# Performance work log

Measured on AMD Instinct MI355X. Metric: run time of the kernel, lower is better.

The kernel has to match this reference:

```python
import jax, jax.numpy as jnp
import numpy as np

N_EMBD = 1024
BLOCK_SIZE = 2048
ATTN_SPAN = 256
LN_EPS = 1e-5


def _band_mask(T, span, dtype):
    ones = jnp.ones((T, T), dtype=dtype)
    # tril(.,0) * (1 - tril(.,-span)) -> causal band of width `span`
    return jnp.tril(ones, 0) * (1.0 - jnp.tril(ones, -span))


def setup_inputs() -> dict:
    key = jax.random.key(0)
    k_x, k_w, k_b, k_lw = jax.random.split(key, 4)
    B, T, C = 4, BLOCK_SIZE, N_EMBD
    x = jax.random.normal(k_x, (B, T, C), dtype=jnp.float32)
    # qkv_net: Linear(C, 3C) with bias (torch default)
    lim = 1.0 / np.sqrt(C)
    W_qkv = jax.random.uniform(k_w, (C, 3 * C), minval=-lim, maxval=lim, dtype=jnp.float32)
    b_qkv = jax.random.uniform(k_b, (3 * C,), minval=-lim, maxval=lim, dtype=jnp.float32)
    ln_w = jnp.ones((C,), dtype=jnp.float32)
    ln_b = jnp.zeros((C,), dtype=jnp.float32)
    return {"x": x, "W_qkv": W_qkv, "b_qkv": b_qkv, "ln_w": ln_w, "ln_b": ln_b}


def _layer_norm(h, w, b):
    mu = jnp.mean(h, axis=-1, keepdims=True)
    var = jnp.var(h, axis=-1, keepdims=True)
    return (h - mu) * jax.lax.rsqrt(var + LN_EPS) * w + b


def reference(x, W_qkv, b_qkv, ln_w, ln_b):
    B, T, C = x.shape
    qkv = x @ W_qkv + b_qkv  # [B,T,3C]
    q, k, v = jnp.split(qkv, 3, axis=-1)
    scale = np.sqrt(C * ATTN_SPAN).astype(np.float32)
    scores = jnp.einsum('bid,bjd->bij', q, k) / scale  # [B,T,T]
    scores = scores * _band_mask(T, ATTN_SPAN, x.dtype)[None, :, :]
    out = jnp.einsum('bij,bjd->bid', scores, v)  # [B,T,C]
    return _layer_norm(out, ln_w, ln_b)
```

## Files before the change

kernel.cpp:

```cpp
#include <hip/hip_runtime.h>
#include <cstdint>
#include <cstddef>

#define N_EMBD 1024
#define T_SEQ  2048
#define NBATCH 4
#define SPAN   256
#define C3     3072

typedef float  floatx4 __attribute__((ext_vector_type(4)));
typedef __bf16 bf16x8  __attribute__((ext_vector_type(8)));

__device__ inline unsigned short f2bf(float f) {
    union { float f; unsigned u; } x; x.f = f;
    unsigned u = x.u;
    unsigned r = (u + 0x7fffu + ((u >> 16) & 1u)) >> 16;
    return (unsigned short)r;
}

typedef __attribute__((address_space(1))) const void GVOID;
typedef __attribute__((address_space(3))) void LVOID;
__device__ inline void gl2lds16(const void* g, void* l) {
    __builtin_amdgcn_global_load_lds((GVOID*)g, (LVOID*)l, 16, 0, 0);
}

__device__ inline void stage128x32(const unsigned short* g, size_t stride,
                                   unsigned short* lds, int lane, int wave) {
    const int r     = wave * 16 + (lane >> 2);
    const int chunk = (lane & 3) ^ ((lane >> 3) & 3);
    const unsigned short* src = g + (size_t)r * stride + chunk * 8;
    gl2lds16(src,               &lds[(wave * 16) * 32]);
    gl2lds16(src + 64 * stride, &lds[(64 + wave * 16) * 32]);
}

__global__ __launch_bounds__(256) void k_prep(const float* __restrict__ x,
                                              unsigned short* __restrict__ Xb,
                                              const float* __restrict__ W,
                                              unsigned short* __restrict__ WbT) {
    __shared__ unsigned short t[32][33];
    if (blockIdx.x < 8192) {
        int i = (blockIdx.x * 256 + threadIdx.x) * 4;
        float4 v = *(const float4*)(x + i);
        ushort4 o;
        o.x = f2bf(v.x); o.y = f2bf(v.y); o.z = f2bf(v.z); o.w = f2bf(v.w);
        *(ushort4*)(Xb + i) = o;
    } else {
        int bid = blockIdx.x - 8192;
        int k0 = (bid & 31) * 32, n0 = (bid >> 5) * 32;
        int tx = threadIdx.x & 31, ty = threadIdx.x >> 5;
#pragma unroll
        for (int i = 0; i < 4; i++) {
            int k = k0 + ty + i * 8;
            t[ty + i * 8][tx] = f2bf(W[(size_t)k * C3 + n0 + tx]);
        }
        __syncthreads();
#pragma unroll
        for (int i = 0; i < 4; i++) {
            int n = n0 + ty + i * 8;
            WbT[(size_t)n * N_EMBD + k0 + tx] = t[tx][ty + i * 8];
        }
    }
}

__global__ __launch_bounds__(256) void k_qkv_gemm(const unsigned short* __restrict__ Xb,
                                                  const unsigned short* __restrict__ WbT,
                                                  const float* __restrict__ bqkv,
                                                  unsigned short* __restrict__ QK,
                                                  unsigned short* __restrict__ Vt) {
    __shared__ unsigned short smem[17408];
    unsigned short* As = smem;
    unsigned short* Bs = smem + 4096;
    const int tid = threadIdx.x, lane = tid & 63, wave = tid >> 6;
    const int n0 = blockIdx.x * 128, m0 = blockIdx.y * 128;
    const int wr = wave >> 1, wc = wave & 1;

    floatx4 acc[4][4] = {};

    const unsigned short* gA = Xb  + (size_t)m0 * N_EMBD;
    const unsigned short* gB = WbT + (size_t)n0 * N_EMBD;
    const int qk = ((lane >> 4) ^ ((lane >> 1) & 3)) * 8;
    const int ra = wr * 64 + (lane & 15);
    const int rb = wc * 64 + (lane & 15);

    for (int k0 = 0; k0 < N_EMBD; k0 += 32) {
        stage128x32(gA + k0, N_EMBD, As, lane, wave);
        stage128x32(gB + k0, N_EMBD, Bs, lane, wave);
        __syncthreads();
        bf16x8 a[4], b[4];
#pragma unroll
        for (int mi = 0; mi < 4; mi++) a[mi] = *(const bf16x8*)&As[(ra + mi * 16) * 32 + qk];
#pragma unroll
        for (int ni = 0; ni < 4; ni++) b[ni] = *(const bf16x8*)&Bs[(rb + ni * 16) * 32 + qk];
#pragma unroll
        for (int mi = 0; mi < 4; mi++)
#pragma unroll
            for (int ni = 0; ni < 4; ni++)
                acc[mi][ni] = __builtin_amdgcn_mfma_f32_16x16x32_bf16(a[mi], b[ni], acc[mi][ni], 0, 0, 0);
        __syncthreads();
    }

    const int cn = lane & 15, q = lane >> 4;
    if (n0 < 2048) {
#pragma unroll
        for (int ni = 0; ni < 4; ni++) {
            const int n = n0 + wc * 64 + ni * 16 + cn;
            const float bias = bqkv[n];
#pragma unroll
            for (int mi = 0; mi < 4; mi++) {
                const int mbase = m0 + wr * 64 + mi * 16 + q * 4;
#pragma unroll
                for (int r = 0; r < 4; r++)
                    QK[(size_t)(mbase + r) * 2048 + n] = f2bf(acc[mi][ni][r] + bias);
            }
        }
    } else {
        unsigned short* tp = smem;
#pragma unroll
        for (int ni = 0; ni < 4; ni++) {
            const int cl = wc * 64 + ni * 16 + cn;
            const float bias = bqkv[n0 + cl];
#pragma unroll
            for (int mi = 0; mi < 4; mi++) {
                const int tl = wr * 64 + mi * 16 + q * 4;
#pragma unroll
                for (int r = 0; r < 4; r++)
                    tp[cl * 136 + tl + r] = f2bf(acc[mi][ni][r] + bias);
            }
        }
        __syncthreads();
        const int clw = tid >> 1, half = tid & 1;
        const int b = m0 >> 11, tg = (m0 & 2047) + half * 64;
        const int cg = n0 - 2048 + clw;
        unsigned short* dst = Vt + ((size_t)(b * 1024 + cg)) * 2048 + tg;
        const unsigned short* src = tp + clw * 136 + half * 64;
#pragma unroll
        for (int i = 0; i < 8; i++)
            *(uint4*)(dst + i * 8) = *(const uint4*)(src + i * 8);
    }
}

__global__ __launch_bounds__(256) void k_scores(const unsigned short* __restrict__ QK,
                                                unsigned short* __restrict__ S) {
    const int jj = blockIdx.x, qb = blockIdx.y, b = blockIdx.z;
    const int jb = qb - 2 + jj;
    if (jb < 0) return;

    __shared__ unsigned short smem[8192];
    unsigned short* As = smem;
    unsigned short* Bs = smem + 4096;
    const int tid = threadIdx.x, lane = tid & 63, wave = tid >> 6;
    const int wr = wave >> 1, wc = wave & 1;

    floatx4 acc[4][4] = {};

    const unsigned short* gQ = QK + ((size_t)(b * T_SEQ + qb * 128)) * 2048;
    const unsigned short* gK = QK + ((size_t)(b * T_SEQ + jb * 128)) * 2048 + 1024;
    const int qk = ((lane >> 4) ^ ((lane >> 1) & 3)) * 8;
    const int ra = wr * 64 + (lane & 15);
    const int rb = wc * 64 + (lane & 15);

    for (int k0 = 0; k0 < N_EMBD; k0 += 32) {
        stage128x32(gQ + k0, 2048, As, lane, wave);
        stage128x32(gK + k0, 2048, Bs, lane, wave);
        __syncthreads();
        bf16x8 a[4], bb[4];
#pragma unroll
        for (int mi = 0; mi < 4; mi++) a[mi]  = *(const bf16x8*)&As[(ra + mi * 16) * 32 + qk];
#pragma unroll
        for (int ni = 0; ni < 4; ni++) bb[ni] = *(const bf16x8*)&Bs[(rb + ni * 16) * 32 + qk];
#pragma unroll
        for (int mi = 0; mi < 4; mi++)
#pragma unroll
            for (int ni = 0; ni < 4; ni++)
                acc[mi][ni] = __builtin_amdgcn_mfma_f32_16x16x32_bf16(a[mi], bb[ni], acc[mi][ni], 0, 0, 0);
        __syncthreads();
    }

    unsigned short* Sb = S + ((size_t)(b * 16 + qb)) * (128 * 384);
    const int cn = lane & 15, q = lane >> 4;
#pragma unroll
    for (int mi = 0; mi < 4; mi++)
#pragma unroll
        for (int ni = 0; ni < 4; ni++)
#pragma unroll
            for (int r = 0; r < 4; r++) {
                const int il = wr * 64 + mi * 16 + q * 4 + r;
                const int jl = wc * 64 + ni * 16 + cn;
                const int gi = qb * 128 + il, gj = jb * 128 + jl;
                const float v = ((gj <= gi) && (gj > gi - SPAN)) ? acc[mi][ni][r] * (1.0f / 512.0f) : 0.0f;
                Sb[il * 384 + jj * 128 + jl] = f2bf(v);
            }
}

__global__ __launch_bounds__(256) void k_sv(const unsigned short* __restrict__ S,
                                            const unsigned short* __restrict__ Vt,
                                            float* __restrict__ out) {
    const int cg = blockIdx.x, qb = blockIdx.y, b = blockIdx.z;
    const int c0 = cg * 128;

    __shared__ unsigned short smem[8192];
    unsigned short* As = smem;
    unsigned short* Bs = smem + 4096;
    const int tid = threadIdx.x, lane = tid & 63, wave = tid >> 6;
    const int wr = wave >> 1, wc = wave & 1;

    floatx4 acc[4][4] = {};

    const unsigned short* Sb = S + ((size_t)(b * 16 + qb)) * (128 * 384);
    const unsigned short* gV = Vt + ((size_t)(b * 1024 + c0)) * 2048;
    const int qk = ((lane >> 4) ^ ((lane >> 1) & 3)) * 8;
    const int ra = wr * 64 + (lane & 15);
    const int rb = wc * 64 + (lane & 15);

    for (int jj = 0; jj < 3; jj++) {
        const int jb = qb - 2 + jj;
        if (jb < 0) continue;
#pragma unroll
        for (int k0 = 0; k0 < 128; k0 += 32) {
            stage128x32(Sb + jj * 128 + k0, 384, As, lane, wave);
            stage128x32(gV + jb * 128 + k0, 2048, Bs, lane, wave);
            __syncthreads();
            bf16x8 a[4], bb[4];
#pragma unroll
            for (int mi = 0; mi < 4; mi++) a[mi]  = *(const bf16x8*)&As[(ra + mi * 16) * 32 + qk];
#pragma unroll
            for (int ni = 0; ni < 4; ni++) bb[ni] = *(const bf16x8*)&Bs[(rb + ni * 16) * 32 + qk];
#pragma unroll
            for (int mi = 0; mi < 4; mi++)
#pragma unroll
                for (int ni = 0; ni < 4; ni++)
                    acc[mi][ni] = __builtin_amdgcn_mfma_f32_16x16x32_bf16(a[mi], bb[ni], acc[mi][ni], 0, 0, 0);
            __syncthreads();
        }
    }

    const int cn = lane & 15, q = lane >> 4;
#pragma unroll
    for (int mi = 0; mi < 4; mi++)
#pragma unroll
        for (int ni = 0; ni < 4; ni++)
#pragma unroll
            for (int r = 0; r < 4; r++) {
                const int il = wr * 64 + mi * 16 + q * 4 + r;
                const int cl = wc * 64 + ni * 16 + cn;
                out[((size_t)(b * T_SEQ + qb * 128 + il)) * N_EMBD + c0 + cl] = acc[mi][ni][r];
            }
}

__global__ __launch_bounds__(256) void k_ln(float* __restrict__ out,
                                            const float* __restrict__ w,
                                            const float* __restrict__ bias) {
    __shared__ float red[8];
    const int t = threadIdx.x;
    float* p = out + (size_t)blockIdx.x * N_EMBD;
    float4 v = ((const float4*)p)[t];
    float s  = v.x + v.y + v.z + v.w;
    float sq = v.x * v.x + v.y * v.y + v.z * v.z + v.w * v.w;
#pragma unroll
    for (int off = 32; off; off >>= 1) {
        s  += __shfl_down(s, off, 64);
        sq += __shfl_down(sq, off, 64);
    }
    const int wave = t >> 6, lane = t & 63;
    if (lane == 0) { red[wave] = s; red[4 + wave] = sq; }
    __syncthreads();
    const float ts = red[0] + red[1] + red[2] + red[3];
    const float tq = red[4] + red[5] + red[6] + red[7];
    const float mean = ts * (1.0f / N_EMBD);
    const float var  = tq * (1.0f / N_EMBD) - mean * mean;
    const float rs = rsqrtf(var + 1e-5f);
    float4 wv = ((const float4*)w)[t];
    float4 bv = ((const float4*)bias)[t];
    float4 o;
    o.x = (v.x - mean) * rs * wv.x + bv.x;
    o.y = (v.y - mean) * rs * wv.y + bv.y;
    o.z = (v.z - mean) * rs * wv.z + bv.z;
    o.w = (v.w - mean) * rs * wv.w + bv.w;
    ((float4*)p)[t] = o;
}

extern "C" void kernel_launch(void* const* d_in, const int* in_sizes, int n_in,
                              void* d_out, int out_size, void* d_ws, size_t ws_size,
                              hipStream_t stream) {
    const float* x  = (const float*)d_in[0];
    const float* W  = (const float*)d_in[1];
    const float* bq = (const float*)d_in[2];
    const float* lw = (const float*)d_in[3];
    const float* lb = (const float*)d_in[4];
    float* out = (float*)d_out;
    char* ws = (char*)d_ws;

    unsigned short* Xb   = (unsigned short*)(ws + 0);
    unsigned short* Sbuf = (unsigned short*)(ws + 0);
    unsigned short* WbT  = (unsigned short*)(ws + 16777216);
    unsigned short* QK   = (unsigned short*)(ws + 23068672);
    unsigned short* Vt   = (unsigned short*)(ws + 56623104);

    k_prep    <<<11264,           256, 0, stream>>>(x, Xb, W, WbT);
    k_qkv_gemm<<<dim3(24, 64),    256, 0, stream>>>(Xb, WbT, bq, QK, Vt);
    k_scores  <<<dim3(3, 16, 4),  256, 0, stream>>>(QK, Sbuf);
    k_sv      <<<dim3(8, 16, 4),  256, 0, stream>>>(Sbuf, Vt, out);
    k_ln      <<<8192,            256, 0, stream>>>(out, lw, lb);
}
```

Baseline: 222.6 us.

## Shrink attention tiles to 64 rows and split QKV GEMM into QK and V kernels

Attention score and SV kernels move from 128-row blocks with 3 key blocks to 64-row blocks with 5 key blocks. This cuts wasted compute on masked band regions and raises the block count for better CU occupancy. The QKV GEMM is split into separate QK and V kernels, and the V transpose now goes through an XOR-swizzled LDS pass done in two halves. New 64-wide staging helpers add swizzling, and the staging chunk swizzle formula changes. The cost is more kernel launches and more, smaller tiles with lower per-block reuse.

```diff
diff --git a/kernel.cpp b/kernel.cpp
--- a/kernel.cpp
+++ b/kernel.cpp
@@ -27,10 +27,30 @@
 __device__ inline void stage128x32(const unsigned short* g, size_t stride,
                                    unsigned short* lds, int lane, int wave) {
     const int r     = wave * 16 + (lane >> 2);
-    const int chunk = (lane & 3) ^ ((lane >> 3) & 3);
+    const int chunk = (lane & 3) ^ ((r >> 1) & 3);
     const unsigned short* src = g + (size_t)r * stride + chunk * 8;
     gl2lds16(src,               &lds[(wave * 16) * 32]);
     gl2lds16(src + 64 * stride, &lds[(64 + wave * 16) * 32]);
+}
+
+__device__ inline void stage64x64(const unsigned short* g, size_t stride,
+                                  unsigned short* lds, int lane, int wave) {
+#pragma unroll
+    for (int rnd = 0; rnd < 2; rnd++) {
+        const int r = rnd * 32 + wave * 8 + (lane >> 3);
+        const int chunk = (lane & 7) ^ (r & 7);
+        gl2lds16(g + (size_t)r * stride + chunk * 8, &lds[(rnd * 32 + wave * 8) * 64]);
+    }
+}
+
+__device__ inline void stage128x64(const unsigned short* g, size_t stride,
+                                   unsigned short* lds, int lane, int wave) {
+#pragma unroll
+    for (int rnd = 0; rnd < 4; rnd++) {
+        const int r = rnd * 32 + wave * 8 + (lane >> 3);
+        const int chunk = (lane & 7) ^ (r & 7);
+        gl2lds16(g + (size_t)r * stride + chunk * 8, &lds[(rnd * 32 + wave * 8) * 64]);
+    }
 }
 
 __global__ __launch_bounds__(256) void k_prep(const float* __restrict__ x,
@@ -62,14 +82,12 @@
     }
 }
 
-__global__ __launch_bounds__(256) void k_qkv_gemm(const unsigned short* __restrict__ Xb,
-                                                  const unsigned short* __restrict__ WbT,
-                                                  const float* __restrict__ bqkv,
-                                                  unsigned short* __restrict__ QK,
-                                                  unsigned short* __restrict__ Vt) {
-    __shared__ unsigned short smem[17408];
-    unsigned short* As = smem;
-    unsigned short* Bs = smem + 4096;
+__global__ __launch_bounds__(256) void k_gemm_qk(const unsigned short* __restrict__ Xb,
+                                                 const unsigned short* __restrict__ WbT,
+                                                 const float* __restrict__ bqkv,
+                                                 unsigned short* __restrict__ QK) {
+    __shared__ unsigned short As[4096];
+    __shared__ unsigned short Bs[4096];
     const int tid = threadIdx.x, lane = tid & 63, wave = tid >> 6;
     const int n0 = blockIdx.x * 128, m0 = blockIdx.y * 128;
     const int wr = wave >> 1, wc = wave & 1;
@@ -100,95 +118,149 @@
     }
 
     const int cn = lane & 15, q = lane >> 4;
-    if (n0 < 2048) {
-#pragma unroll
-        for (int ni = 0; ni < 4; ni++) {
-            const int n = n0 + wc * 64 + ni * 16 + cn;
-            const float bias = bqkv[n];
-#pragma unroll
-            for (int mi = 0; mi < 4; mi++) {
-                const int mbase = m0 + wr * 64 + mi * 16 + q * 4;
-#pragma unroll
-                for (int r = 0; r < 4; r++)
-                    QK[(size_t)(mbase + r) * 2048 + n] = f2bf(acc[mi][ni][r] + bias);
-            }
-        }
-    } else {
-        unsigned short* tp = smem;
-#pragma unroll
-        for (int ni = 0; ni < 4; ni++) {
-            const int cl = wc * 64 + ni * 16 + cn;
-            const float bias = bqkv[n0 + cl];
-#pragma unroll
-            for (int mi = 0; mi < 4; mi++) {
-                const int tl = wr * 64 + mi * 16 + q * 4;
-#pragma unroll
-                for (int r = 0; r < 4; r++)
-                    tp[cl * 136 + tl + r] = f2bf(acc[mi][ni][r] + bias);
-            }
-        }
-        __syncthreads();
-        const int clw = tid >> 1, half = tid & 1;
-        const int b = m0 >> 11, tg = (m0 & 2047) + half * 64;
-        const int cg = n0 - 2048 + clw;
-        unsigned short* dst = Vt + ((size_t)(b * 1024 + cg)) * 2048 + tg;
-        const unsigned short* src = tp + clw * 136 + half * 64;
-#pragma unroll
-        for (int i = 0; i < 8; i++)
-            *(uint4*)(dst + i * 8) = *(const uint4*)(src + i * 8);
-    }
-}
-
-__global__ __launch_bounds__(256) void k_scores(const unsigned short* __restrict__ QK,
-                                                unsigned short* __restrict__ S) {
-    const int jj = blockIdx.x, qb = blockIdx.y, b = blockIdx.z;
-    const int jb = qb - 2 + jj;
-    if (jb < 0) return;
-
+#pragma unroll
+    for (int ni = 0; ni < 4; ni++) {
+        const int n = n0 + wc * 64 + ni * 16 + cn;
+        const float bias = bqkv[n];
+#pragma unroll
+        for (int mi = 0; mi < 4; mi++) {
+            const int mbase = m0 + wr * 64 + mi * 16 + q * 4;
+#pragma unroll
+            for (int r = 0; r < 4; r++)
+                QK[(size_t)(mbase + r) * 2048 + n] = f2bf(acc[mi][ni][r] + bias);
+        }
+    }
+}
+
+__global__ __launch_bounds__(256) void k_gemm_v(const unsigned short* __restrict__ Xb,
+                                                const unsigned short* __restrict__ WbT,
+                                                const float* __restrict__ bqkv,
+                                                unsigned short* __restrict__ Vt) {
     __shared__ unsigned short smem[8192];
     unsigned short* As = smem;
     unsigned short* Bs = smem + 4096;
     const int tid = threadIdx.x, lane = tid & 63, wave = tid >> 6;
+    const int n0 = 2048 + blockIdx.x * 128, m0 = blockIdx.y * 128;
     const int wr = wave >> 1, wc = wave & 1;
 
     floatx4 acc[4][4] = {};
 
-    const unsigned short* gQ = QK + ((size_t)(b * T_SEQ + qb * 128)) * 2048;
-    const unsigned short* gK = QK + ((size_t)(b * T_SEQ + jb * 128)) * 2048 + 1024;
+    const unsigned short* gA = Xb  + (size_t)m0 * N_EMBD;
+    const unsigned short* gB = WbT + (size_t)n0 * N_EMBD;
     const int qk = ((lane >> 4) ^ ((lane >> 1) & 3)) * 8;
     const int ra = wr * 64 + (lane & 15);
     const int rb = wc * 64 + (lane & 15);
 
     for (int k0 = 0; k0 < N_EMBD; k0 += 32) {
-        stage128x32(gQ + k0, 2048, As, lane, wave);
-        stage128x32(gK + k0, 2048, Bs, lane, wave);
-        __syncthreads();
-        bf16x8 a[4], bb[4];
-#pragma unroll
-        for (int mi = 0; mi < 4; mi++) a[mi]  = *(const bf16x8*)&As[(ra + mi * 16) * 32 + qk];
-#pragma unroll
-        for (int ni = 0; ni < 4; ni++) bb[ni] = *(const bf16x8*)&Bs[(rb + ni * 16) * 32 + qk];
+        stage128x32(gA + k0, N_EMBD, As, lane, wave);
+        stage128x32(gB + k0, N_EMBD, Bs, lane, wave);
+        __syncthreads();
+        bf16x8 a[4], b[4];
+#pragma unroll
+        for (int mi = 0; mi < 4; mi++) a[mi] = *(const bf16x8*)&As[(ra + mi * 16) * 32 + qk];
+#pragma unroll
+        for (int ni = 0; ni < 4; ni++) b[ni] = *(const bf16x8*)&Bs[(rb + ni * 16) * 32 + qk];
 #pragma unroll
         for (int mi = 0; mi < 4; mi++)
 #pragma unroll
             for (int ni = 0; ni < 4; ni++)
-                acc[mi][ni] = __builtin_amdgcn_mfma_f32_16x16x32_bf16(a[mi], bb[ni], acc[mi][ni], 0, 0, 0);
-        __syncthreads();
-    }
-
-    unsigned short* Sb = S + ((size_t)(b * 16 + qb)) * (128 * 384);
+                acc[mi][ni] = __builtin_amdgcn_mfma_f32_16x16x32_bf16(a[mi], b[ni], acc[mi][ni], 0, 0, 0);
+        __syncthreads();
+    }
+
+    unsigned short* tp = smem;
     const int cn = lane & 15, q = lane >> 4;
-#pragma unroll
-    for (int mi = 0; mi < 4; mi++)
-#pragma unroll
-        for (int ni = 0; ni < 4; ni++)
+    const int bb = m0 >> 11, tg0 = m0 & 2047, cb = n0 - 2048;
+#pragma unroll
+    for (int p = 0; p < 2; p++) {
+        if (p) __syncthreads();
+        if (wc == p) {
+#pragma unroll
+            for (int ni = 0; ni < 4; ni++) {
+                const int cl = ni * 16 + cn;
+                const float bias = bqkv[n0 + p * 64 + cl];
+#pragma unroll
+                for (int mi = 0; mi < 4; mi++) {
+                    const int t0 = wr * 64 + mi * 16 + q * 4;
+#pragma unroll
+                    for (int r = 0; r < 4; r += 2) {
+                        const unsigned lo = f2bf(acc[mi][ni][r] + bias);
+                        const unsigned hi = f2bf(acc[mi][ni][r + 1] + bias);
+                        const int t = t0 + r;
+                        const int idx = cl * 128 + (((t >> 3) ^ (cl & 7)) * 8) + (t & 7);
+                        *(unsigned*)&tp[idx] = lo | (hi << 16);
+                    }
+                }
+            }
+        }
+        __syncthreads();
+        const int row = tid >> 2;
+        const int key = row & 7;
+        unsigned short* dst = Vt + ((size_t)(bb * 1024 + cb + p * 64 + row)) * 2048 + tg0;
+#pragma unroll
+        for (int i = 0; i < 4; i++) {
+            const int ch = (tid & 3) + i * 4;
+            uint4 d = *(const uint4*)&tp[row * 128 + ((ch ^ key) * 8)];
+            *(uint4*)(dst + ch * 8) = d;
+        }
+    }
+}
+
+__global__ __launch_bounds__(256) void k_scores(const unsigned short* __restrict__ QK,
+                                                unsigned short* __restrict__ S) {
+    const int jj = blockIdx.x, qb = blockIdx.y, b = blockIdx.z;
+    const int jb = qb - 4 + jj;
+    if (jb < 0) return;
+
+    __shared__ unsigned short Qs[4096];
+    __shared__ unsigned short Ks[4096];
+    const int tid = threadIdx.x, lane = tid & 63, wave = tid >> 6;
+    const int wr = wave >> 1, wc = wave & 1;
+    const int n15 = lane & 15, q = lane >> 4;
+
+    floatx4 acc[2][2] = {};
+
+    const unsigned short* gQ = QK + ((size_t)(b * T_SEQ + qb * 64)) * 2048;
+    const unsigned short* gK = QK + ((size_t)(b * T_SEQ + jb * 64)) * 2048 + 1024;
+
+    for (int k0 = 0; k0 < N_EMBD; k0 += 64) {
+        stage64x64(gQ + k0, 2048, Qs, lane, wave);
+        stage64x64(gK + k0, 2048, Ks, lane, wave);
+        __syncthreads();
+#pragma unroll
+        for (int s = 0; s < 2; s++) {
+            bf16x8 a[2], bbf[2];
+#pragma unroll
+            for (int mi = 0; mi < 2; mi++) {
+                const int row = wr * 32 + mi * 16 + n15;
+                a[mi] = *(const bf16x8*)&Qs[row * 64 + (((s * 4 + q) ^ (row & 7)) * 8)];
+            }
+#pragma unroll
+            for (int ni = 0; ni < 2; ni++) {
+                const int row = wc * 32 + ni * 16 + n15;
+                bbf[ni] = *(const bf16x8*)&Ks[row * 64 + (((s * 4 + q) ^ (row & 7)) * 8)];
+            }
+#pragma unroll
+            for (int mi = 0; mi < 2; mi++)
+#pragma unroll
+                for (int ni = 0; ni < 2; ni++)
+                    acc[mi][ni] = __builtin_amdgcn_mfma_f32_16x16x32_bf16(a[mi], bbf[ni], acc[mi][ni], 0, 0, 0);
+        }
+        __syncthreads();
+    }
+
+    unsigned short* Sb = S + (((size_t)(b * 32 + qb) * 5 + jj) << 12);
+#pragma unroll
+    for (int mi = 0; mi < 2; mi++)
+#pragma unroll
+        for (int ni = 0; ni < 2; ni++)
 #pragma unroll
             for (int r = 0; r < 4; r++) {
-                const int il = wr * 64 + mi * 16 + q * 4 + r;
-                const int jl = wc * 64 + ni * 16 + cn;
-                const int gi = qb * 128 + il, gj = jb * 128 + jl;
+                const int il = wr * 32 + mi * 16 + q * 4 + r;
+                const int jl = wc * 32 + ni * 16 + n15;
+                const int gi = qb * 64 + il, gj = jb * 64 + jl;
                 const float v = ((gj <= gi) && (gj > gi - SPAN)) ? acc[mi][ni][r] * (1.0f / 512.0f) : 0.0f;
-                Sb[il * 384 + jj * 128 + jl] = f2bf(v);
+                Sb[il * 64 + jl] = f2bf(v);
             }
 }
 
@@ -198,52 +270,51 @@
     const int cg = blockIdx.x, qb = blockIdx.y, b = blockIdx.z;
     const int c0 = cg * 128;
 
-    __shared__ unsigned short smem[8192];
-    unsigned short* As = smem;
-    unsigned short* Bs = smem + 4096;
+    __shared__ unsigned short Ss[4096];
+    __shared__ unsigned short Vs[8192];
     const int tid = threadIdx.x, lane = tid & 63, wave = tid >> 6;
     const int wr = wave >> 1, wc = wave & 1;
-
-    floatx4 acc[4][4] = {};
-
-    const unsigned short* Sb = S + ((size_t)(b * 16 + qb)) * (128 * 384);
-    const unsigned short* gV = Vt + ((size_t)(b * 1024 + c0)) * 2048;
-    const int qk = ((lane >> 4) ^ ((lane >> 1) & 3)) * 8;
-    const int ra = wr * 64 + (lane & 15);
-    const int rb = wc * 64 + (lane & 15);
-
-    for (int jj = 0; jj < 3; jj++) {
-        const int jb = qb - 2 + jj;
+    const int n15 = lane & 15, q = lane >> 4;
+
+    floatx4 acc[2][4] = {};
+
+    for (int jj = 0; jj < 5; jj++) {
+        const int jb = qb - 4 + jj;
         if (jb < 0) continue;
-#pragma unroll
-        for (int k0 = 0; k0 < 128; k0 += 32) {
-            stage128x32(Sb + jj * 128 + k0, 384, As, lane, wave);
-            stage128x32(gV + jb * 128 + k0, 2048, Bs, lane, wave);
-            __syncthreads();
-            bf16x8 a[4], bb[4];
-#pragma unroll
-            for (int mi = 0; mi < 4; mi++) a[mi]  = *(const bf16x8*)&As[(ra + mi * 16) * 32 + qk];
-#pragma unroll
-            for (int ni = 0; ni < 4; ni++) bb[ni] = *(const bf16x8*)&Bs[(rb + ni * 16) * 32 + qk];
-#pragma unroll
-            for (int mi = 0; mi < 4; mi++)
+        stage64x64(S + (((size_t)(b * 32 + qb) * 5 + jj) << 12), 64, Ss, lane, wave);
+        stage128x64(Vt + ((size_t)(b * 1024 + c0)) * 2048 + jb * 64, 2048, Vs, lane, wave);
+        __syncthreads();
+#pragma unroll
+        for (int s = 0; s < 2; s++) {
+            bf16x8 a[2], bbf[4];
+#pragma unroll
+            for (int mi = 0; mi < 2; mi++) {
+                const int row = wr * 32 + mi * 16 + n15;
+                a[mi] = *(const bf16x8*)&Ss[row * 64 + (((s * 4 + q) ^ (row & 7)) * 8)];
+            }
+#pragma unroll
+            for (int ni = 0; ni < 4; ni++) {
+                const int row = wc * 64 + ni * 16 + n15;
+                bbf[ni] = *(const bf16x8*)&Vs[row * 64 + (((s * 4 + q) ^ (row & 7)) * 8)];
+            }
+#pragma unroll
+            for (int mi = 0; mi < 2; mi++)
 #pragma unroll
                 for (int ni = 0; ni < 4; ni++)
-                    acc[mi][ni] = __builtin_amdgcn_mfma_f32_16x16x32_bf16(a[mi], bb[ni], acc[mi][ni], 0, 0, 0);
-            __syncthreads();
-        }
-    }
-
-    const int cn = lane & 15, q = lane >> 4;
-#pragma unroll
-    for (int mi = 0; mi < 4; mi++)
+                    acc[mi][ni] = __builtin_amdgcn_mfma_f32_16x16x32_bf16(a[mi], bbf[ni], acc[mi][ni], 0, 0, 0);
+        }
+        __syncthreads();
+    }
+
+#pragma unroll
+    for (int mi = 0; mi < 2; mi++)
 #pragma unroll
         for (int ni = 0; ni < 4; ni++)
 #pragma unroll
             for (int r = 0; r < 4; r++) {
-                const int il = wr * 64 + mi * 16 + q * 4 + r;
-                const int cl = wc * 64 + ni * 16 + cn;
-                out[((size_t)(b * T_SEQ + qb * 128 + il)) * N_EMBD + c0 + cl] = acc[mi][ni][r];
+                const int il = wr * 32 + mi * 16 + q * 4 + r;
+                const int cl = wc * 64 + ni * 16 + n15;
+                out[((size_t)(b * T_SEQ + qb * 64 + il)) * N_EMBD + c0 + cl] = acc[mi][ni][r];
             }
 }
 
@@ -297,8 +368,9 @@
     unsigned short* Vt   = (unsigned short*)(ws + 56623104);
 
     k_prep    <<<11264,           256, 0, stream>>>(x, Xb, W, WbT);
-    k_qkv_gemm<<<dim3(24, 64),    256, 0, stream>>>(Xb, WbT, bq, QK, Vt);
-    k_scores  <<<dim3(3, 16, 4),  256, 0, stream>>>(QK, Sbuf);
-    k_sv      <<<dim3(8, 16, 4),  256, 0, stream>>>(Sbuf, Vt, out);
+    k_gemm_qk <<<dim3(16, 64),    256, 0, stream>>>(Xb, WbT, bq, QK);
+    k_gemm_v  <<<dim3(8, 64),     256, 0, stream>>>(Xb, WbT, bq, Vt);
+    k_scores  <<<dim3(5, 32, 4),  256, 0, stream>>>(QK, Sbuf);
+    k_sv      <<<dim3(8, 32, 4),  256, 0, stream>>>(Sbuf, Vt, out);
     k_ln      <<<8192,            256, 0, stream>>>(out, lw, lb);
 }
```

Result: no change. 220.5 us (-1.0%).
